# Kernel optimization log

Measured on AMD Instinct MI355X. Metric: run time of the kernel, lower is better.

The kernel has to match this reference:

```python
import jax, jax.numpy as jnp
import numpy as np

D_MODEL = 1024
H = 16
BLOCK_SIZE = 64
STRIDE = 64
CAUSAL = False


def create_sparse_mask(T, block_size, stride, causal):
    i = jnp.arange(T)[:, None]
    j = jnp.arange(T)[None, :]
    same_block = (i // block_size) == (j // block_size)
    strided = ((i - j) % stride) == 0
    allow = same_block | strided
    if causal:
        allow = allow & (j <= i)
    return allow  # [T, T] bool


def setup_inputs() -> dict:
    key = jax.random.key(0)
    ks = jax.random.split(key, 7)
    B, T, D = 1, 4096, D_MODEL
    scale = 1.0 / np.sqrt(D)
    return {
        "q": jax.random.normal(ks[0], (B, T, D), jnp.float32),
        "k": jax.random.normal(ks[1], (B, T, D), jnp.float32),
        "v": jax.random.normal(ks[2], (B, T, D), jnp.float32),
        "mask": jnp.ones((B, T, T), dtype=bool),
        "Wq": jax.random.normal(ks[3], (D, D), jnp.float32) * scale,
        "Wk": jax.random.normal(ks[4], (D, D), jnp.float32) * scale,
        "Wv": jax.random.normal(ks[5], (D, D), jnp.float32) * scale,
        "Wo": jax.random.normal(ks[6], (D, D), jnp.float32) * scale,
    }


def reference(q, k, v, mask, Wq, Wk, Wv, Wo):
    # NOTE: the original module computes Q, K, V all from the first arg `q`;
    # k and v inputs are accepted but unused (faithful reproduction).
    B, T, D = q.shape
    h, dk = H, D // H

    def proj(x, W):  # nn.Linear(bias=False): x @ W.T -> [B, h, T, dk]
        return (x @ W.T).reshape(B, T, h, dk).transpose(0, 2, 1, 3)

    qh, kh, vh = proj(q, Wq), proj(q, Wk), proj(q, Wv)

    sparse = create_sparse_mask(T, BLOCK_SIZE, STRIDE, CAUSAL)  # [T, T]
    attn_mask = sparse[None, None, :, :] & mask[:, None, :, :]  # [B, h(broadcast), T, T]

    scores = jnp.einsum("bhqd,bhkd->bhqk", qh, kh) / np.sqrt(dk)
    scores = jnp.where(attn_mask, scores, -jnp.inf)
    attn = jax.nn.softmax(scores, axis=-1)  # dropout p=0.0 -> identity
    out = jnp.einsum("bhqk,bhkd->bhqd", attn, vh)
    out = out.transpose(0, 2, 1, 3).reshape(B, T, D)
    return out @ Wo.T
```

## Files before the change

### kernel.cpp

```cpp
#include <hip/hip_runtime.h>
#include <stdint.h>

typedef __attribute__((ext_vector_type(8))) short bf16x8;
typedef __attribute__((ext_vector_type(4))) float f32x4;
typedef __attribute__((ext_vector_type(4))) unsigned short us4;
typedef __attribute__((ext_vector_type(8))) unsigned short us8;

static __device__ __forceinline__ unsigned short f2bf(float f) {
  unsigned u = __float_as_uint(f);
  u = (u + 0x7FFFu + ((u >> 16) & 1u)) >> 16;
  return (unsigned short)u;
}
static __device__ __forceinline__ float bf2f(unsigned short u) {
  return __uint_as_float(((unsigned)u) << 16);
}

#define MFMA16(a, b, c) __builtin_amdgcn_mfma_f32_16x16x32_bf16((a), (b), (c), 0, 0, 0)

#define GLL16(g, l)                                                             \
  __builtin_amdgcn_global_load_lds(                                             \
      (__attribute__((address_space(1))) unsigned int*)(uintptr_t)(g),          \
      (__attribute__((address_space(3))) unsigned int*)(uintptr_t)(l), 16, 0, 0)

__global__ void prep_kernel(const float* __restrict__ q,
                            const float* __restrict__ Wq,
                            const float* __restrict__ Wk,
                            const float* __restrict__ Wv,
                            const float* __restrict__ Wo,
                            unsigned short* __restrict__ Xb,
                            unsigned short* __restrict__ Wqkv,
                            unsigned short* __restrict__ Wob) {
  const int bid = blockIdx.x;
  const int c = threadIdx.x * 4;
  const float* src;
  unsigned short* dst;
  float scale = 1.f;
  if (bid < 4096) {
    src = q + (long)bid * 1024;
    dst = Xb + (long)bid * 1024;
  } else if (bid < 7168) {
    const int w = bid - 4096;
    src = ((w < 1024) ? Wq : (w < 2048) ? Wk : Wv) + (long)(w & 1023) * 1024;
    dst = Wqkv + (long)w * 1024;
    if (w < 1024) scale = 0.125f;
  } else {
    const int w = bid - 7168;
    src = Wo + (long)w * 1024;
    dst = Wob + (long)w * 1024;
  }
  float4 x = *(const float4*)(src + c);
  float xs[4] = {x.x * scale, x.y * scale, x.z * scale, x.w * scale};
  us4 hi;
#pragma unroll
  for (int i = 0; i < 4; i++) hi[i] = f2bf(xs[i]);
  *(us4*)(dst + c) = hi;
}

__global__ __launch_bounds__(256) void gemm_bt_bf16(
    const unsigned short* __restrict__ A, const unsigned short* __restrict__ B,
    float* __restrict__ C, int K, int N) {
  __shared__ __align__(16) unsigned short As[128 * 32];
  __shared__ __align__(16) unsigned short Bs[128 * 32];
  const int bm = blockIdx.x, bn = blockIdx.y;
  const int tid = threadIdx.x;
  const int wave = tid >> 6, lane = tid & 63;
  const int wr = wave >> 1, wc = wave & 1;

  f32x4 zero = {0.f, 0.f, 0.f, 0.f};
  f32x4 acc[4][4];
#pragma unroll
  for (int m = 0; m < 4; m++)
#pragma unroll
    for (int n = 0; n < 4; n++) acc[m][n] = zero;

  const int srow = wave * 16 + (lane >> 2);
  const int skof = (lane & 3) * 8;
  const unsigned short* Ab = A + (size_t)(bm * 128 + srow) * K + skof;
  const unsigned short* Bb = B + (size_t)(bn * 128 + srow) * K + skof;
  const size_t rstep = (size_t)64 * K;
  unsigned short* AsW = As + wave * 512;
  unsigned short* BsW = Bs + wave * 512;

  const int fr = lane & 15;
  const int fk = (lane >> 4) * 8;

  for (int k0 = 0; k0 < K; k0 += 32) {
    if (k0) __syncthreads();
#pragma unroll
    for (int i = 0; i < 2; i++) {
      GLL16(Ab + i * rstep + k0, AsW + i * 2048);
      GLL16(Bb + i * rstep + k0, BsW + i * 2048);
    }
    __syncthreads();
    bf16x8 af[4], bv[4];
#pragma unroll
    for (int m = 0; m < 4; m++)
      af[m] = *(const bf16x8*)&As[(wr * 64 + m * 16 + fr) * 32 + fk];
#pragma unroll
    for (int n = 0; n < 4; n++)
      bv[n] = *(const bf16x8*)&Bs[(wc * 64 + n * 16 + fr) * 32 + fk];
#pragma unroll
    for (int m = 0; m < 4; m++)
#pragma unroll
      for (int n = 0; n < 4; n++) acc[m][n] = MFMA16(af[m], bv[n], acc[m][n]);
  }

  const int crow = bm * 128 + wr * 64 + (lane >> 4) * 4;
  const int ccol = bn * 128 + wc * 64 + (lane & 15);
#pragma unroll
  for (int m = 0; m < 4; m++)
#pragma unroll
    for (int n = 0; n < 4; n++)
#pragma unroll
      for (int r = 0; r < 4; r++)
        C[(size_t)(crow + m * 16 + r) * N + ccol + n * 16] = acc[m][n][r];
}

__device__ __forceinline__ void stage_half(unsigned short* lds_tile,
                                           const unsigned short* gbase,
                                           int k0, int half, int tid) {
#pragma unroll
  for (int i = 0; i < 2; i++) {
    const int c = i * 512 + tid;
    const int r = c >> 3;
    const int j = c & 7;
    const int js = j ^ (r & 7);
    const unsigned short* g = gbase + (size_t)(half * 128 + r) * 1024 + k0 + js * 8;
    unsigned short* l = lds_tile + half * 8192 + (i * 512 + (tid & ~63)) * 8;
    GLL16(g, l);
  }
}

__global__ __launch_bounds__(512, 2) void gemm256_bt(
    const unsigned short* __restrict__ A, const unsigned short* __restrict__ B,
    unsigned short* __restrict__ C) {
  const int NT = 16;
  __shared__ __align__(16) unsigned short AS[2][16384];
  __shared__ __align__(16) unsigned short BS[2][16384];
  const int wg = blockIdx.x;
  const int swz = (wg & 7) * 24 + (wg >> 3);
  const int bm = swz / 12, bn = swz % 12;
  const int tid = threadIdx.x;
  const int wave = tid >> 6, lane = tid & 63;
  const int wm = wave >> 2, wn = wave & 3;

  const unsigned short* Ag = A + (size_t)bm * 256 * 1024;
  const unsigned short* Bg = B + (size_t)bn * 256 * 1024;

  f32x4 zero = {0.f, 0.f, 0.f, 0.f};
  f32x4 acc[8][4];
#pragma unroll
  for (int m = 0; m < 8; m++)
#pragma unroll
    for (int n = 0; n < 4; n++) acc[m][n] = zero;

  stage_half(AS[0], Ag, 0, 0, tid);
  stage_half(AS[0], Ag, 0, 1, tid);
  stage_half(BS[0], Bg, 0, 0, tid);
  stage_half(BS[0], Bg, 0, 1, tid);
  stage_half(BS[1], Bg, 64, 0, tid);
  stage_half(BS[1], Bg, 64, 1, tid);
  stage_half(AS[1], Ag, 64, 0, tid);
  asm volatile("s_waitcnt vmcnt(6)" ::: "memory");
  __builtin_amdgcn_s_barrier();

  const int fr = lane & 15;
  const int fko = (lane >> 4) * 8;

  for (int t = 0; t < NT; t++) {
    const int cur = t & 1;
    const unsigned short* At = AS[cur];
    const unsigned short* Bt = BS[cur];
    bf16x8 av[4][2], bv[4][2];

#pragma unroll
    for (int m = 0; m < 4; m++) {
      const int row = wm * 128 + m * 16 + fr;
      const int sw = (row & 7) << 3;
      av[m][0] = *(const bf16x8*)&At[row * 64 + (fko ^ sw)];
      av[m][1] = *(const bf16x8*)&At[row * 64 + ((32 + fko) ^ sw)];
    }
#pragma unroll
    for (int n = 0; n < 2; n++) {
      const int row = wn * 64 + n * 16 + fr;
      const int sw = (row & 7) << 3;
      bv[n][0] = *(const bf16x8*)&Bt[row * 64 + (fko ^ sw)];
      bv[n][1] = *(const bf16x8*)&Bt[row * 64 + ((32 + fko) ^ sw)];
    }
    if (t + 1 < NT) stage_half(AS[cur ^ 1], Ag, (t + 1) * 64, 1, tid);
    __builtin_amdgcn_s_barrier();
    __builtin_amdgcn_s_setprio(1);
#pragma unroll
    for (int m = 0; m < 4; m++)
#pragma unroll
      for (int n = 0; n < 2; n++) {
        acc[m][n] = MFMA16(av[m][0], bv[n][0], acc[m][n]);
        acc[m][n] = MFMA16(av[m][1], bv[n][1], acc[m][n]);
      }
    __builtin_amdgcn_s_setprio(0);
    __builtin_amdgcn_s_barrier();

#pragma unroll
    for (int n = 2; n < 4; n++) {
      const int row = wn * 64 + n * 16 + fr;
      const int sw = (row & 7) << 3;
      bv[n][0] = *(const bf16x8*)&Bt[row * 64 + (fko ^ sw)];
      bv[n][1] = *(const bf16x8*)&Bt[row * 64 + ((32 + fko) ^ sw)];
    }
    __builtin_amdgcn_s_barrier();
    __builtin_amdgcn_s_setprio(1);
#pragma unroll
    for (int m = 0; m < 4; m++)
#pragma unroll
      for (int n = 2; n < 4; n++) {
        acc[m][n] = MFMA16(av[m][0], bv[n][0], acc[m][n]);
        acc[m][n] = MFMA16(av[m][1], bv[n][1], acc[m][n]);
      }
    __builtin_amdgcn_s_setprio(0);
    __builtin_amdgcn_s_barrier();

#pragma unroll
    for (int m = 0; m < 4; m++) {
      const int row = wm * 128 + (m + 4) * 16 + fr;
      const int sw = (row & 7) << 3;
      av[m][0] = *(const bf16x8*)&At[row * 64 + (fko ^ sw)];
      av[m][1] = *(const bf16x8*)&At[row * 64 + ((32 + fko) ^ sw)];
    }
    if (t + 2 < NT) stage_half(BS[cur], Bg, (t + 2) * 64, 0, tid);
    __builtin_amdgcn_s_barrier();
    __builtin_amdgcn_s_setprio(1);
#pragma unroll
    for (int m = 0; m < 4; m++)
#pragma unroll
      for (int n = 0; n < 2; n++) {
        acc[m + 4][n] = MFMA16(av[m][0], bv[n][0], acc[m + 4][n]);
        acc[m + 4][n] = MFMA16(av[m][1], bv[n][1], acc[m + 4][n]);
      }
    __builtin_amdgcn_s_setprio(0);
    __builtin_amdgcn_s_barrier();

    if (t + 2 < NT) {
      stage_half(BS[cur], Bg, (t + 2) * 64, 1, tid);
      stage_half(AS[cur], Ag, (t + 2) * 64, 0, tid);
    }
    __builtin_amdgcn_s_barrier();
    __builtin_amdgcn_s_setprio(1);
#pragma unroll
    for (int m = 0; m < 4; m++)
#pragma unroll
      for (int n = 2; n < 4; n++) {
        acc[m + 4][n] = MFMA16(av[m][0], bv[n][0], acc[m + 4][n]);
        acc[m + 4][n] = MFMA16(av[m][1], bv[n][1], acc[m + 4][n]);
      }
    __builtin_amdgcn_s_setprio(0);
    if (t < NT - 1) {
      if (t + 2 < NT)
        asm volatile("s_waitcnt vmcnt(6)" ::: "memory");
      else
        asm volatile("s_waitcnt vmcnt(0)" ::: "memory");
      __builtin_amdgcn_s_barrier();
    }
  }

  const int crow = bm * 256 + wm * 128 + (lane >> 4) * 4;
  const int ccol = bn * 256 + wn * 64 + (lane & 15);
#pragma unroll
  for (int m = 0; m < 8; m++)
#pragma unroll
    for (int n = 0; n < 4; n++)
#pragma unroll
      for (int r = 0; r < 4; r++)
        C[(size_t)(crow + m * 16 + r) * 3072 + ccol + n * 16] =
            f2bf(acc[m][n][r]);
}

__global__ __launch_bounds__(256) void attn_kernel(
    const unsigned short* __restrict__ QKV, unsigned short* __restrict__ O0,
    unsigned short* __restrict__ O1, float2* __restrict__ St0,
    float2* __restrict__ St1) {
  __shared__ __align__(16) unsigned short QP[64 * 64];
  __shared__ __align__(16) unsigned short Ks[64 * 64];
  __shared__ __align__(16) unsigned short Vt[64 * 64];
  __shared__ __align__(16) float Sf[64 * 68];
  const int bid = blockIdx.x;
  const int f = bid >> 10, h = (bid >> 6) & 15, t = bid & 63;
  const int tid = threadIdx.x;
  const int wave = tid >> 6, lane = tid & 63;

  {
#pragma unroll
    for (int i = 0; i < 2; i++) {
      const int c = i * 256 + tid;
      const int row = c >> 3;
      const int ch = c & 7;
      const int js = ch ^ (row & 7);
      const long grow = f ? ((long)row * 64 + t) : ((long)t * 64 + row);
      const unsigned short* gq = QKV + grow * 3072 + h * 64 + js * 8;
      const int ldof = i * 2048 + (wave << 9);
      GLL16(gq, QP + ldof);
      GLL16(gq + 1024, Ks + ldof);
    }
  }
  {
    const int j = tid >> 2;
    const int d0 = (tid & 3) * 16;
    const long grow = f ? ((long)j * 64 + t) : ((long)t * 64 + j);
    const unsigned short* vsrc = QKV + grow * 3072 + 2048 + h * 64 + d0;
#pragma unroll
    for (int e = 0; e < 16; e += 8) {
      bf16x8 v8 = *(const bf16x8*)(vsrc + e);
#pragma unroll
      for (int c = 0; c < 8; c++) {
        const int d = d0 + e + c;
        Vt[d * 64 + (j ^ ((d & 7) << 3))] = (unsigned short)v8[c];
      }
    }
  }
  __syncthreads();

  const int wr = wave >> 1, wc = wave & 1;
  const int fr = lane & 15;
  const int fko = (lane >> 4) * 8;
  f32x4 zero = {0.f, 0.f, 0.f, 0.f};

  {
    f32x4 acc[2][2] = {{zero, zero}, {zero, zero}};
#pragma unroll
    for (int s = 0; s < 2; s++) {
      bf16x8 av[2], bv[2];
#pragma unroll
      for (int m = 0; m < 2; m++) {
        const int row = wr * 32 + m * 16 + fr;
        const int kk = (s * 32 + fko) ^ ((row & 7) << 3);
        av[m] = *(const bf16x8*)&QP[row * 64 + kk];
      }
#pragma unroll
      for (int n = 0; n < 2; n++) {
        const int row = wc * 32 + n * 16 + fr;
        const int kk = (s * 32 + fko) ^ ((row & 7) << 3);
        bv[n] = *(const bf16x8*)&Ks[row * 64 + kk];
      }
#pragma unroll
      for (int m = 0; m < 2; m++)
#pragma unroll
        for (int n = 0; n < 2; n++) acc[m][n] = MFMA16(av[m], bv[n], acc[m][n]);
    }
    const int r0 = wr * 32 + (lane >> 4) * 4;
    const int c0 = wc * 32 + (lane & 15);
#pragma unroll
    for (int m = 0; m < 2; m++)
#pragma unroll
      for (int n = 0; n < 2; n++)
#pragma unroll
        for (int r = 0; r < 4; r++)
          Sf[(r0 + m * 16 + r) * 68 + c0 + n * 16] = acc[m][n][r];
  }
  __syncthreads();

  {
    const int qrow = tid >> 2;
    const int sub = tid & 3;
    float s[16];
#pragma unroll
    for (int e = 0; e < 4; e++) {
      float4 v = *(const float4*)&Sf[qrow * 68 + sub * 16 + e * 4];
      s[e * 4 + 0] = v.x;
      s[e * 4 + 1] = v.y;
      s[e * 4 + 2] = v.z;
      s[e * 4 + 3] = v.w;
    }
    float mx = s[0];
#pragma unroll
    for (int e = 1; e < 16; e++) mx = fmaxf(mx, s[e]);
    mx = fmaxf(mx, __shfl_xor(mx, 1, 64));
    mx = fmaxf(mx, __shfl_xor(mx, 2, 64));
    float ev[16];
    float z = 0.f;
#pragma unroll
    for (int e = 0; e < 16; e++) {
      float v = __expf(s[e] - mx);
      if (f == 1 && (sub * 16 + e) == qrow) v = 0.f;
      ev[e] = v;
      z += v;
    }
    z += __shfl_xor(z, 1, 64);
    z += __shfl_xor(z, 2, 64);
    const float inv = 1.f / z;
    __attribute__((aligned(16))) unsigned short pb[16];
#pragma unroll
    for (int e = 0; e < 16; e++) pb[e] = f2bf(ev[e] * inv);
#pragma unroll
    for (int cc = 0; cc < 2; cc++) {
      const int chunk = (sub * 2 + cc) ^ (qrow & 7);
      *(us8*)&QP[qrow * 64 + chunk * 8] = *(const us8*)&pb[cc * 8];
    }
    if (sub == 0) {
      const long qg = f ? ((long)qrow * 64 + t) : ((long)t * 64 + qrow);
      (f ? St1 : St0)[(long)h * 4096 + qg] = make_float2(mx, z);
    }
  }
  __syncthreads();

  f32x4 acc[2][2] = {{zero, zero}, {zero, zero}};
#pragma unroll
  for (int s = 0; s < 2; s++) {
    bf16x8 av[2], bv[2];
#pragma unroll
    for (int m = 0; m < 2; m++) {
      const int row = wr * 32 + m * 16 + fr;
      const int kk = (s * 32 + fko) ^ ((row & 7) << 3);
      av[m] = *(const bf16x8*)&QP[row * 64 + kk];
    }
#pragma unroll
    for (int n = 0; n < 2; n++) {
      const int row = wc * 32 + n * 16 + fr;
      const int kk = (s * 32 + fko) ^ ((row & 7) << 3);
      bv[n] = *(const bf16x8*)&Vt[row * 64 + kk];
    }
#pragma unroll
    for (int m = 0; m < 2; m++)
#pragma unroll
      for (int n = 0; n < 2; n++) acc[m][n] = MFMA16(av[m], bv[n], acc[m][n]);
  }
  const int r0 = wr * 32 + (lane >> 4) * 4;
  const int c0 = wc * 32 + (lane & 15);
  if (f == 0) {
#pragma unroll
    for (int m = 0; m < 2; m++)
#pragma unroll
      for (int n = 0; n < 2; n++)
#pragma unroll
        for (int r = 0; r < 4; r++)
          O0[((long)t * 64 + r0 + m * 16 + r) * 1024 + h * 64 + c0 + n * 16] =
              f2bf(acc[m][n][r]);
  } else {
#pragma unroll
    for (int m = 0; m < 2; m++)
#pragma unroll
      for (int n = 0; n < 2; n++)
#pragma unroll
        for (int r = 0; r < 4; r++)
          O1[(((long)h * 64 + t) * 64 + r0 + m * 16 + r) * 64 + c0 + n * 16] =
              f2bf(acc[m][n][r]);
  }
}

__global__ void combine_kernel(const unsigned short* __restrict__ O0,
                               const unsigned short* __restrict__ O1,
                               const float2* __restrict__ St0,
                               const float2* __restrict__ St1,
                               unsigned short* __restrict__ Ot) {
  const int i = blockIdx.x;
  const int c = threadIdx.x * 4;
  const int h = c >> 6, d = c & 63, b = i >> 6, r = i & 63;
  us4 n0 = *(const us4*)(O0 + (long)i * 1024 + c);
  us4 n1 = *(const us4*)(O1 + (((long)h * 64 + r) * 64 + b) * 64 + d);
  float2 s0 = St0[(long)h * 4096 + i];
  float2 s1 = St1[(long)h * 4096 + i];
  const float M = fmaxf(s0.x, s1.x);
  const float w0 = __expf(s0.x - M) * s0.y;
  const float w1 = __expf(s1.x - M) * s1.y;
  const float inv = 1.f / (w0 + w1);
  const float a0 = w0 * inv, a1 = w1 * inv;
  us4 hi;
#pragma unroll
  for (int e = 0; e < 4; e++)
    hi[e] = f2bf(a0 * bf2f(n0[e]) + a1 * bf2f(n1[e]));
  *(us4*)(Ot + (long)i * 1024 + c) = hi;
}

extern "C" void kernel_launch(void* const* d_in, const int* in_sizes, int n_in,
                              void* d_out, int out_size, void* d_ws,
                              size_t ws_size, hipStream_t stream) {
  const float* q = (const float*)d_in[0];
  const float* Wq = (const float*)d_in[4];
  const float* Wk = (const float*)d_in[5];
  const float* Wv = (const float*)d_in[6];
  const float* Wo = (const float*)d_in[7];
  float* out = (float*)d_out;

  char* ws = (char*)d_ws;
  unsigned short* Xb = (unsigned short*)(ws);
  unsigned short* Ot = (unsigned short*)(ws);
  unsigned short* Wqkv = (unsigned short*)(ws + 8388608);
  unsigned short* Wob = (unsigned short*)(ws + 14680064);
  unsigned short* QKVb = (unsigned short*)(ws + 16777216);
  unsigned short* O0 = (unsigned short*)(ws + 41943040);
  unsigned short* O1 = (unsigned short*)(ws + 50331648);
  float2* St0 = (float2*)(ws + 58720256);
  float2* St1 = (float2*)(ws + 59244544);

  prep_kernel<<<8192, 256, 0, stream>>>(q, Wq, Wk, Wv, Wo, Xb, Wqkv, Wob);

  gemm256_bt<<<192, 512, 0, stream>>>(Xb, Wqkv, QKVb);

  attn_kernel<<<2048, 256, 0, stream>>>(QKVb, O0, O1, St0, St1);
  combine_kernel<<<4096, 256, 0, stream>>>(O0, O1, St0, St1, Ot);

  gemm_bt_bf16<<<dim3(32, 8), 256, 0, stream>>>(Ot, Wob, out, 1024, 1024);
}
```

Baseline: 90.36 us.

## Fuse split-softmax combine into output projection GEMM A-tile loading

Removes the separate combine kernel and folds the merging of the two partial attention outputs (rescaling by softmax statistics) into the A-operand staging of the output projection GEMM. Each GEMM block loads O0/O1 and the stats, computes the weighted combination in registers, and writes bf16 directly to LDS, which avoids one kernel launch and the round trip of the combined tensor through global memory. In exchange, the combine work is repeated across the 8 column blocks, and A loads become synchronous register loads instead of async global-to-LDS copies. The strided O1 reads are also less coalesced.

```diff
diff --git a/kernel.cpp b/kernel.cpp
--- a/kernel.cpp
+++ b/kernel.cpp
@@ -56,66 +56,6 @@
   *(us4*)(dst + c) = hi;
 }
 
-__global__ __launch_bounds__(256) void gemm_bt_bf16(
-    const unsigned short* __restrict__ A, const unsigned short* __restrict__ B,
-    float* __restrict__ C, int K, int N) {
-  __shared__ __align__(16) unsigned short As[128 * 32];
-  __shared__ __align__(16) unsigned short Bs[128 * 32];
-  const int bm = blockIdx.x, bn = blockIdx.y;
-  const int tid = threadIdx.x;
-  const int wave = tid >> 6, lane = tid & 63;
-  const int wr = wave >> 1, wc = wave & 1;
-
-  f32x4 zero = {0.f, 0.f, 0.f, 0.f};
-  f32x4 acc[4][4];
-#pragma unroll
-  for (int m = 0; m < 4; m++)
-#pragma unroll
-    for (int n = 0; n < 4; n++) acc[m][n] = zero;
-
-  const int srow = wave * 16 + (lane >> 2);
-  const int skof = (lane & 3) * 8;
-  const unsigned short* Ab = A + (size_t)(bm * 128 + srow) * K + skof;
-  const unsigned short* Bb = B + (size_t)(bn * 128 + srow) * K + skof;
-  const size_t rstep = (size_t)64 * K;
-  unsigned short* AsW = As + wave * 512;
-  unsigned short* BsW = Bs + wave * 512;
-
-  const int fr = lane & 15;
-  const int fk = (lane >> 4) * 8;
-
-  for (int k0 = 0; k0 < K; k0 += 32) {
-    if (k0) __syncthreads();
-#pragma unroll
-    for (int i = 0; i < 2; i++) {
-      GLL16(Ab + i * rstep + k0, AsW + i * 2048);
-      GLL16(Bb + i * rstep + k0, BsW + i * 2048);
-    }
-    __syncthreads();
-    bf16x8 af[4], bv[4];
-#pragma unroll
-    for (int m = 0; m < 4; m++)
-      af[m] = *(const bf16x8*)&As[(wr * 64 + m * 16 + fr) * 32 + fk];
-#pragma unroll
-    for (int n = 0; n < 4; n++)
-      bv[n] = *(const bf16x8*)&Bs[(wc * 64 + n * 16 + fr) * 32 + fk];
-#pragma unroll
-    for (int m = 0; m < 4; m++)
-#pragma unroll
-      for (int n = 0; n < 4; n++) acc[m][n] = MFMA16(af[m], bv[n], acc[m][n]);
-  }
-
-  const int crow = bm * 128 + wr * 64 + (lane >> 4) * 4;
-  const int ccol = bn * 128 + wc * 64 + (lane & 15);
-#pragma unroll
-  for (int m = 0; m < 4; m++)
-#pragma unroll
-    for (int n = 0; n < 4; n++)
-#pragma unroll
-      for (int r = 0; r < 4; r++)
-        C[(size_t)(crow + m * 16 + r) * N + ccol + n * 16] = acc[m][n][r];
-}
-
 __device__ __forceinline__ void stage_half(unsigned short* lds_tile,
                                            const unsigned short* gbase,
                                            int k0, int half, int tid) {
@@ -445,28 +385,82 @@
   }
 }
 
-__global__ void combine_kernel(const unsigned short* __restrict__ O0,
-                               const unsigned short* __restrict__ O1,
-                               const float2* __restrict__ St0,
-                               const float2* __restrict__ St1,
-                               unsigned short* __restrict__ Ot) {
-  const int i = blockIdx.x;
-  const int c = threadIdx.x * 4;
-  const int h = c >> 6, d = c & 63, b = i >> 6, r = i & 63;
-  us4 n0 = *(const us4*)(O0 + (long)i * 1024 + c);
-  us4 n1 = *(const us4*)(O1 + (((long)h * 64 + r) * 64 + b) * 64 + d);
-  float2 s0 = St0[(long)h * 4096 + i];
-  float2 s1 = St1[(long)h * 4096 + i];
-  const float M = fmaxf(s0.x, s1.x);
-  const float w0 = __expf(s0.x - M) * s0.y;
-  const float w1 = __expf(s1.x - M) * s1.y;
-  const float inv = 1.f / (w0 + w1);
-  const float a0 = w0 * inv, a1 = w1 * inv;
-  us4 hi;
-#pragma unroll
-  for (int e = 0; e < 4; e++)
-    hi[e] = f2bf(a0 * bf2f(n0[e]) + a1 * bf2f(n1[e]));
-  *(us4*)(Ot + (long)i * 1024 + c) = hi;
+__global__ __launch_bounds__(256) void out_gemm_fused(
+    const unsigned short* __restrict__ O0, const unsigned short* __restrict__ O1,
+    const float2* __restrict__ St0, const float2* __restrict__ St1,
+    const unsigned short* __restrict__ B, float* __restrict__ C) {
+  __shared__ __align__(16) unsigned short As[128 * 32];
+  __shared__ __align__(16) unsigned short Bs[128 * 32];
+  const int bm = blockIdx.x, bn = blockIdx.y;
+  const int tid = threadIdx.x;
+  const int wave = tid >> 6, lane = tid & 63;
+  const int wr = wave >> 1, wc = wave & 1;
+
+  f32x4 zero = {0.f, 0.f, 0.f, 0.f};
+  f32x4 acc[4][4];
+#pragma unroll
+  for (int m = 0; m < 4; m++)
+#pragma unroll
+    for (int n = 0; n < 4; n++) acc[m][n] = zero;
+
+  const int srow = wave * 16 + (lane >> 2);
+  const int skof = (lane & 3) * 8;
+  const unsigned short* Bb = B + (size_t)(bn * 128 + srow) * 1024 + skof;
+  const size_t rstep = (size_t)64 * 1024;
+  unsigned short* BsW = Bs + wave * 512;
+
+  const int fr = lane & 15;
+  const int fk = (lane >> 4) * 8;
+
+  for (int k0 = 0; k0 < 1024; k0 += 32) {
+    if (k0) __syncthreads();
+    const int h = k0 >> 6;
+    const int d0 = (k0 + skof) & 63;
+#pragma unroll
+    for (int i = 0; i < 2; i++) {
+      GLL16(Bb + i * rstep + k0, BsW + i * 2048);
+      const int gi = bm * 128 + srow + i * 64;
+      const int b = gi >> 6, r = gi & 63;
+      us8 o0 = *(const us8*)(O0 + (long)gi * 1024 + h * 64 + d0);
+      us8 o1 = *(const us8*)(O1 + (((long)h * 64 + r) * 64 + b) * 64 + d0);
+      const float2 s0 = St0[(long)h * 4096 + gi];
+      const float2 s1 = St1[(long)h * 4096 + gi];
+      const float M = fmaxf(s0.x, s1.x);
+      const float w0 = __expf(s0.x - M) * s0.y;
+      const float w1 = __expf(s1.x - M) * s1.y;
+      const float inv = 1.f / (w0 + w1);
+      const float a0 = w0 * inv, a1 = w1 * inv;
+      us8 av;
+#pragma unroll
+      for (int e = 0; e < 8; e++)
+        av[e] = f2bf(f2bf(a0 * bf2f(o0[e]) + a1 * bf2f(o1[e])) == 0
+                         ? a0 * bf2f(o0[e]) + a1 * bf2f(o1[e])
+                         : a0 * bf2f(o0[e]) + a1 * bf2f(o1[e]));
+      *(us8*)&As[i * 2048 + srow * 32 + skof] = av;
+    }
+    __syncthreads();
+    bf16x8 af[4], bv[4];
+#pragma unroll
+    for (int m = 0; m < 4; m++)
+      af[m] = *(const bf16x8*)&As[(wr * 64 + m * 16 + fr) * 32 + fk];
+#pragma unroll
+    for (int n = 0; n < 4; n++)
+      bv[n] = *(const bf16x8*)&Bs[(wc * 64 + n * 16 + fr) * 32 + fk];
+#pragma unroll
+    for (int m = 0; m < 4; m++)
+#pragma unroll
+      for (int n = 0; n < 4; n++) acc[m][n] = MFMA16(af[m], bv[n], acc[m][n]);
+  }
+
+  const int crow = bm * 128 + wr * 64 + (lane >> 4) * 4;
+  const int ccol = bn * 128 + wc * 64 + (lane & 15);
+#pragma unroll
+  for (int m = 0; m < 4; m++)
+#pragma unroll
+    for (int n = 0; n < 4; n++)
+#pragma unroll
+      for (int r = 0; r < 4; r++)
+        C[(size_t)(crow + m * 16 + r) * 1024 + ccol + n * 16] = acc[m][n][r];
 }
 
 extern "C" void kernel_launch(void* const* d_in, const int* in_sizes, int n_in,
@@ -481,7 +475,6 @@
 
   char* ws = (char*)d_ws;
   unsigned short* Xb = (unsigned short*)(ws);
-  unsigned short* Ot = (unsigned short*)(ws);
   unsigned short* Wqkv = (unsigned short*)(ws + 8388608);
   unsigned short* Wob = (unsigned short*)(ws + 14680064);
   unsigned short* QKVb = (unsigned short*)(ws + 16777216);
@@ -495,7 +488,6 @@
   gemm256_bt<<<192, 512, 0, stream>>>(Xb, Wqkv, QKVb);
 
   attn_kernel<<<2048, 256, 0, stream>>>(QKVb, O0, O1, St0, St1);
-  combine_kernel<<<4096, 256, 0, stream>>>(O0, O1, St0, St1, Ot);
-
-  gemm_bt_bf16<<<dim3(32, 8), 256, 0, stream>>>(Ot, Wob, out, 1024, 1024);
-}
+
+  out_gemm_fused<<<dim3(32, 8), 256, 0, stream>>>(O0, O1, St0, St1, Wob, out);
+}
```

Measured after the change: 102.1 us. 13.0% more time.
